# Performance work log

Measured on AMD Instinct MI355X. Metric: run time of the kernel, lower is better.

## Reference

```python
import jax, jax.numpy as jnp
import numpy as np
import math

B, N, DIM = 2, 4096, 256
NUM_HEADS = 8
HEAD_DIM = DIM // NUM_HEADS
WINDOW = 7  # default window_size in create_local_mask


def local_mask(seq_len: int, window_size: int = WINDOW) -> jnp.ndarray:
    """Boolean [N,N] mask: True where attention is allowed (2D grid locality)."""
    grid = int(math.isqrt(seq_len))
    idx = jnp.arange(seq_len)
    row, col = idx // grid, idx % grid
    half = window_size // 2
    ok_row = jnp.abs(row[:, None] - row[None, :]) <= half
    ok_col = jnp.abs(col[:, None] - col[None, :]) <= half
    return ok_row & ok_col


def setup_inputs() -> dict:
    key = jax.random.key(0)
    k1, k2, k3, k4 = jax.random.split(key, 4)
    x = jax.random.normal(k1, (B, N, DIM), dtype=jnp.float32)
    W_qkv = jax.random.normal(k2, (3 * DIM, DIM), dtype=jnp.float32) * (DIM ** -0.5)
    W_proj = jax.random.normal(k3, (DIM, DIM), dtype=jnp.float32) * (DIM ** -0.5)
    b_proj = jax.random.normal(k4, (DIM,), dtype=jnp.float32) * 0.01
    temperature = jnp.ones((1,), dtype=jnp.float32)
    return {"x": x, "W_qkv": W_qkv, "W_proj": W_proj, "b_proj": b_proj,
            "temperature": temperature}


def reference(x, W_qkv, W_proj, b_proj, temperature):
    Bb, Nn, C = x.shape
    scale = HEAD_DIM ** -0.5
    # qkv linear (no bias): [B,N,3C] -> [3,B,H,N,hd]
    qkv = (x @ W_qkv.T).reshape(Bb, Nn, 3, NUM_HEADS, HEAD_DIM)
    qkv = jnp.transpose(qkv, (2, 0, 3, 1, 4))
    q, k, v = qkv[0], qkv[1], qkv[2]
    # scores with learnable temperature
    attn = jnp.einsum('bhqd,bhkd->bhqk', q, k) * (scale * temperature[0])
    mask = local_mask(Nn)  # training path: N > 100 -> mask applied
    attn = jnp.where(mask[None, None, :, :], attn, -jnp.inf)
    attn = jax.nn.softmax(attn, axis=-1)
    out = jnp.einsum('bhqk,bhkd->bhqd', attn, v)  # [B,H,N,hd]
    out = jnp.transpose(out, (0, 2, 1, 3)).reshape(Bb, Nn, C)
    return out @ W_proj.T + b_proj
```

## Files before the change

### kernel.cpp

```cpp
#include <hip/hip_runtime.h>
#include <hip/hip_bf16.h>
#include <math.h>

#define DIM   256
#define NHEAD 8
#define HD    32
#define NTOK  4096
#define GRD   64
#define BATCH 2
#define MTOT  (BATCH * NTOK)
#define PLANE (NTOK * HD)

typedef __attribute__((ext_vector_type(8))) short bf16x8;
typedef __attribute__((ext_vector_type(4))) float f32x4;

static __device__ __forceinline__ unsigned short f2b(float f) {
  __hip_bfloat16 h = __float2bfloat16(f);
  union { __hip_bfloat16 h; unsigned short u; } cv;
  cv.h = h;
  return cv.u;
}

static __device__ __forceinline__ unsigned cvtpk_bf16(float lo, float hi) {
  unsigned r;
  asm("v_cvt_pk_bf16_f32 %0, %1, %2" : "=v"(r) : "v"(lo), "v"(hi));
  return r;
}

static __device__ __forceinline__ bf16x8 pack8(float4 a0, float4 a1) {
  union { bf16x8 v; unsigned short u[8]; } o;
  o.u[0] = f2b(a0.x); o.u[1] = f2b(a0.y); o.u[2] = f2b(a0.z); o.u[3] = f2b(a0.w);
  o.u[4] = f2b(a1.x); o.u[5] = f2b(a1.y); o.u[6] = f2b(a1.z); o.u[7] = f2b(a1.w);
  return o.v;
}

#define GLDS16(SRC, DST) __builtin_amdgcn_global_load_lds( \
    (const __attribute__((address_space(1))) void*)(SRC),  \
    (__attribute__((address_space(3))) void*)(DST), 16, 0, 0)

__global__ __launch_bounds__(256) void gemm_qkv(const float* __restrict__ A,
                                                const float* __restrict__ Bw,
                                                unsigned short* __restrict__ Cout) {
  const int K = 256;
  __shared__ __align__(16) char smem[34816];
  __hip_bfloat16* As = (__hip_bfloat16*)smem;
  __hip_bfloat16* Bs = (__hip_bfloat16*)(smem + 10240);
  const int tid = threadIdx.x;
  const int l = tid & 63, w = tid >> 6;
  const int bm = blockIdx.y * 128, bn = blockIdx.x * 128;
  const int wr = w >> 1, wc = w & 1;
  const int lr = l & 15, kh = l >> 4;
  const int lrow = l >> 2, lcol = (l & 3) * 8;

  f32x4 acc[4][4];
  #pragma unroll
  for (int i = 0; i < 4; ++i)
    #pragma unroll
    for (int j = 0; j < 4; ++j)
      acc[i][j] = (f32x4){0.f, 0.f, 0.f, 0.f};

  for (int k0 = 0; k0 < K; k0 += 32) {
    #pragma unroll
    for (int i = 0; i < 2; ++i) {
      const int r0 = (w * 2 + i) * 16;
      const float* ga = A  + (size_t)(bm + r0 + lrow) * K + k0 + lcol;
      const float* gb = Bw + (size_t)(bn + r0 + lrow) * K + k0 + lcol;
      float4 a0 = *(const float4*)ga, a1 = *(const float4*)(ga + 4);
      float4 b0 = *(const float4*)gb, b1 = *(const float4*)(gb + 4);
      *(bf16x8*)&As[(r0 + lrow) * 40 + lcol] = pack8(a0, a1);
      *(bf16x8*)&Bs[(r0 + lrow) * 40 + lcol] = pack8(b0, b1);
    }
    __syncthreads();

    bf16x8 af[4], bfr[4];
    #pragma unroll
    for (int f = 0; f < 4; ++f) {
      af[f]  = *(const bf16x8*)&As[(wr * 64 + f * 16 + lr) * 40 + kh * 8];
      bfr[f] = *(const bf16x8*)&Bs[(wc * 64 + f * 16 + lr) * 40 + kh * 8];
    }
    #pragma unroll
    for (int fi = 0; fi < 4; ++fi)
      #pragma unroll
      for (int fj = 0; fj < 4; ++fj)
        acc[fi][fj] = __builtin_amdgcn_mfma_f32_16x16x32_bf16(af[fi], bfr[fj], acc[fi][fj], 0, 0, 0);
    __syncthreads();
  }

  if (blockIdx.x < 4) {
    #pragma unroll
    for (int fi = 0; fi < 4; ++fi)
      #pragma unroll
      for (int fj = 0; fj < 4; ++fj)
        #pragma unroll
        for (int rr = 0; rr < 4; ++rr) {
          const int m = bm + wr * 64 + fi * 16 + kh * 4 + rr;
          const int n = bn + wc * 64 + fj * 16 + lr;
          const int sel = n >> 8, rem = n & 255;
          const int hh = rem >> 5, d = rem & 31;
          const int bb = m >> 12, tok = m & 4095;
          Cout[(size_t)(sel * 16 + bb * 8 + hh) * PLANE + tok * 32 + d] =
              f2b(acc[fi][fj][rr]);
        }
  } else {
    unsigned short* Ts = (unsigned short*)smem;
    #pragma unroll
    for (int fi = 0; fi < 4; ++fi)
      #pragma unroll
      for (int fj = 0; fj < 4; ++fj)
        #pragma unroll
        for (int rr = 0; rr < 4; ++rr) {
          const int tokl = wr * 64 + fi * 16 + kh * 4 + rr;
          const int dl   = wc * 64 + fj * 16 + lr;
          Ts[tokl * 136 + dl] = f2b(acc[fi][fj][rr]);
        }
    __syncthreads();
    const int dl = tid >> 1, th = (tid & 1) * 64;
    const int dg = (bn - 512) + dl;
    const int hh = dg >> 5, dd = dg & 31;
    const int bb = bm >> 12, tokb = bm & 4095;
    unsigned short* vt = Cout + (size_t)(32 + bb * 8 + hh) * PLANE + dd * 4096 + tokb + th;
    #pragma unroll
    for (int j = 0; j < 8; ++j) {
      union { bf16x8 v; unsigned short u[8]; } o;
      #pragma unroll
      for (int e = 0; e < 8; ++e)
        o.u[e] = Ts[(th + j * 8 + e) * 136 + dl];
      *(bf16x8*)(vt + j * 8) = o.v;
    }
  }
}

__global__ __launch_bounds__(256) void gemm_proj(const __hip_bfloat16* __restrict__ A,
                                                 const float* __restrict__ Bw,
                                                 const float* __restrict__ bias,
                                                 float* __restrict__ Cout) {
  const int K = 256, N = 256;
  __shared__ __hip_bfloat16 As[128 * 32];
  __shared__ __hip_bfloat16 Bs[128 * 40];
  const int tid = threadIdx.x;
  const int l = tid & 63, w = tid >> 6;
  const int bm = blockIdx.y * 128, bn = blockIdx.x * 128;
  const int wr = w >> 1, wc = w & 1;
  const int lr = l & 15, kh = l >> 4;
  const int lrow = l >> 2, lcol = (l & 3) * 8;

  f32x4 acc[4][4];
  #pragma unroll
  for (int i = 0; i < 4; ++i)
    #pragma unroll
    for (int j = 0; j < 4; ++j)
      acc[i][j] = (f32x4){0.f, 0.f, 0.f, 0.f};

  for (int k0 = 0; k0 < K; k0 += 32) {
    #pragma unroll
    for (int i = 0; i < 2; ++i) {
      const int r0 = (w * 2 + i) * 16;
      const __hip_bfloat16* ga = A + (size_t)(bm + r0 + lrow) * K + k0 + lcol;
      GLDS16(ga, &As[r0 * 32]);
      const float* gb = Bw + (size_t)(bn + r0 + lrow) * K + k0 + lcol;
      float4 b0 = *(const float4*)gb, b1 = *(const float4*)(gb + 4);
      *(bf16x8*)&Bs[(r0 + lrow) * 40 + lcol] = pack8(b0, b1);
    }
    __syncthreads();

    bf16x8 af[4], bfr[4];
    #pragma unroll
    for (int f = 0; f < 4; ++f) {
      af[f]  = *(const bf16x8*)&As[(wr * 64 + f * 16 + lr) * 32 + kh * 8];
      bfr[f] = *(const bf16x8*)&Bs[(wc * 64 + f * 16 + lr) * 40 + kh * 8];
    }
    #pragma unroll
    for (int fi = 0; fi < 4; ++fi)
      #pragma unroll
      for (int fj = 0; fj < 4; ++fj)
        acc[fi][fj] = __builtin_amdgcn_mfma_f32_16x16x32_bf16(af[fi], bfr[fj], acc[fi][fj], 0, 0, 0);
    __syncthreads();
  }

  #pragma unroll
  for (int fi = 0; fi < 4; ++fi)
    #pragma unroll
    for (int fj = 0; fj < 4; ++fj)
      #pragma unroll
      for (int rr = 0; rr < 4; ++rr) {
        const int m = bm + wr * 64 + fi * 16 + kh * 4 + rr;
        const int n = bn + wc * 64 + fj * 16 + lr;
        Cout[(size_t)m * N + n] = acc[fi][fj][rr] + bias[n];
      }
}

__global__ __launch_bounds__(256) void local_attn_mfma(
    const unsigned short* __restrict__ qkv, const float* __restrict__ temp,
    unsigned short* __restrict__ attn_out) {
  __shared__ __align__(16) unsigned short Ks[448 * 32];
  __shared__ __align__(16) unsigned short Vt[32 * 512];

  const int P = blockIdx.x;
  const int L = (P & 7) * 128 + (P >> 3);
  const int b = L >> 9, h = (L >> 6) & 7, r = L & 63;
  const int tid = threadIdx.x;
  const int l = tid & 63, wv = tid >> 6;
  const int q15 = l & 15, sg = l >> 4;

  const float scale = 0.17677669529663687f * temp[0];

  const unsigned short* qplane  = qkv + (size_t)(b * 8 + h) * PLANE;
  const unsigned short* kplane  = qplane + (size_t)16 * PLANE;
  const unsigned short* vtplane = qplane + (size_t)32 * PLANE;

  #pragma unroll
  for (int i = 0; i < 7; ++i) {
    const int ch = i * 256 + tid;
    const int tok = ch >> 2, jjp = ch & 3;
    const int ri = tok >> 6, kloc = tok & 63;
    int rr = r - 3 + ri; rr = rr < 0 ? 0 : (rr > 63 ? 63 : rr);
    const int jl = jjp ^ ((tok >> 1) & 3);
    const unsigned short* src = kplane + (size_t)(rr * 64 + kloc) * 32 + jl * 8;
    GLDS16(src, &Ks[(i * 256 + (tid & ~63)) * 8]);
  }
  #pragma unroll
  for (int i = 0; i < 8; ++i) {
    const int ch = i * 256 + tid;
    const int d = ch >> 6, chp = ch & 63;
    const int chl = chp ^ (d & 7);
    const int ri = chl >> 3, part = chl & 7;
    int rr = r - 3 + ri; rr = rr < 0 ? 0 : (rr > 63 ? 63 : rr);
    const unsigned short* src = vtplane + (size_t)d * 4096 + rr * 64 + part * 8;
    GLDS16(src, &Vt[(i * 256 + (tid & ~63)) * 8]);
  }

  const bf16x8 qf = *(const bf16x8*)(qplane + (size_t)(r * 64 + wv * 16 + q15) * 32 + sg * 8);

  __syncthreads();

  const int qcol = wv * 16 + q15;
  float m_run = -INFINITY, l_run = 0.f;
  f32x4 Od[2];
  Od[0] = (f32x4){0.f, 0.f, 0.f, 0.f};
  Od[1] = (f32x4){0.f, 0.f, 0.f, 0.f};
  const f32x4 zf = {0.f, 0.f, 0.f, 0.f};
  const int laA = ((l >> 4) & 1) * 32 + q15;
  const int laB = laA + 16;
  const bool hiG = (l & 32) != 0;

  #pragma unroll
  for (int c = 0; c < 7; ++c) {
    const int rr_c = r - 3 + c;
    if (rr_c >= 0 && rr_c <= 63) {
      f32x4 st[4];
      #pragma unroll
      for (int kt = 0; kt < 4; ++kt) {
        const int tok = c * 64 + kt * 16 + q15;
        const bf16x8 kf = *(const bf16x8*)((const char*)Ks + tok * 64 +
                                           ((sg ^ ((tok >> 1) & 3)) << 4));
        st[kt] = __builtin_amdgcn_mfma_f32_16x16x32_bf16(kf, qf, zf, 0, 0, 0);
      }
      float mc = -INFINITY;
      #pragma unroll
      for (int kt = 0; kt < 4; ++kt)
        #pragma unroll
        for (int rg = 0; rg < 4; ++rg) {
          const int keyloc = kt * 16 + sg * 4 + rg;
          const bool ok = (unsigned)(keyloc - qcol + 3) <= 6u;
          const float v = ok ? st[kt][rg] * scale : -INFINITY;
          st[kt][rg] = v;
          mc = fmaxf(mc, v);
        }
      mc = fmaxf(mc, __shfl_xor(mc, 16));
      mc = fmaxf(mc, __shfl_xor(mc, 32));
      const float mnew = fmaxf(m_run, mc);
      const float alpha = __expf(m_run - mnew);
      float lc = 0.f;
      #pragma unroll
      for (int kt = 0; kt < 4; ++kt)
        #pragma unroll
        for (int rg = 0; rg < 4; ++rg) {
          const float e = __expf(st[kt][rg] - mnew);
          st[kt][rg] = e;
          lc += e;
        }
      lc += __shfl_xor(lc, 16);
      lc += __shfl_xor(lc, 32);
      l_run = l_run * alpha + lc;
      m_run = mnew;
      Od[0] *= alpha;
      Od[1] *= alpha;

      unsigned pkw[8];
      #pragma unroll
      for (int kt = 0; kt < 4; ++kt) {
        pkw[kt * 2 + 0] = cvtpk_bf16(st[kt][0], st[kt][1]);
        pkw[kt * 2 + 1] = cvtpk_bf16(st[kt][2], st[kt][3]);
      }
      #pragma unroll
      for (int hf = 0; hf < 2; ++hf) {
        unsigned wA[2], wB[2];
        #pragma unroll
        for (int w2 = 0; w2 < 2; ++w2) {
          const unsigned a0 = (unsigned)__shfl((int)pkw[(2 * hf) * 2 + w2], laA);
          const unsigned a1 = (unsigned)__shfl((int)pkw[(2 * hf + 1) * 2 + w2], laA);
          wA[w2] = hiG ? a1 : a0;
          const unsigned b0 = (unsigned)__shfl((int)pkw[(2 * hf) * 2 + w2], laB);
          const unsigned b1 = (unsigned)__shfl((int)pkw[(2 * hf + 1) * 2 + w2], laB);
          wB[w2] = hiG ? b1 : b0;
        }
        union { unsigned u[4]; bf16x8 v; } pf;
        pf.u[0] = wA[0]; pf.u[1] = wA[1]; pf.u[2] = wB[0]; pf.u[3] = wB[1];
        #pragma unroll
        for (int dt = 0; dt < 2; ++dt) {
          const int d = dt * 16 + q15;
          const int chl = c * 8 + hf * 4 + sg;
          const bf16x8 vf = *(const bf16x8*)((const char*)Vt + d * 1024 +
                                             ((chl ^ (d & 7)) << 4));
          Od[dt] = __builtin_amdgcn_mfma_f32_16x16x32_bf16(vf, pf.v, Od[dt], 0, 0, 0);
        }
      }
    }
  }

  const float invl = 1.0f / l_run;
  #pragma unroll
  for (int dt = 0; dt < 2; ++dt) {
    const unsigned w0 = cvtpk_bf16(Od[dt][0] * invl, Od[dt][1] * invl);
    const unsigned w1 = cvtpk_bf16(Od[dt][2] * invl, Od[dt][3] * invl);
    unsigned short* dst = attn_out + (size_t)(b * 4096 + r * 64 + qcol) * 256 +
                          h * 32 + dt * 16 + sg * 4;
    uint2 uu; uu.x = w0; uu.y = w1;
    *(uint2*)dst = uu;
  }
}

extern "C" void kernel_launch(void* const* d_in, const int* in_sizes, int n_in,
                              void* d_out, int out_size, void* d_ws, size_t ws_size,
                              hipStream_t stream) {
  const float* x     = (const float*)d_in[0];
  const float* Wqkv  = (const float*)d_in[1];
  const float* Wproj = (const float*)d_in[2];
  const float* bproj = (const float*)d_in[3];
  const float* temp  = (const float*)d_in[4];
  float* out = (float*)d_out;

  char* ws = (char*)d_ws;
  unsigned short* qkv_bf  = (unsigned short*)ws;
  __hip_bfloat16* attn_bf = (__hip_bfloat16*)(ws + 25165824);

  {
    dim3 grid(3 * DIM / 128, MTOT / 128);
    gemm_qkv<<<grid, 256, 0, stream>>>(x, Wqkv, qkv_bf);
  }
  local_attn_mfma<<<BATCH * NHEAD * GRD, 256, 0, stream>>>(qkv_bf, temp,
                                                           (unsigned short*)attn_bf);
  {
    dim3 grid(DIM / 128, MTOT / 128);
    gemm_proj<<<grid, 256, 0, stream>>>(attn_bf, Wproj, bproj, out);
  }
}
```

Before: 50.64 us.

## Process two query rows per attention block and shrink proj GEMM M-tile

The attention kernel now uses 512-thread blocks that each handle two adjacent query grid rows and share a single 8-row K/V window in LDS. Previously each 256-thread block loaded its own 7-row window, so this cuts redundant global loads and halves the grid. The output projection GEMM switches from 128-row to 64-row tiles, doubling its block count so more CUs are busy on the small problem. The cost is more LDS per attention block and less operand reuse per proj block.

```diff
diff --git a/kernel.cpp b/kernel.cpp
--- a/kernel.cpp
+++ b/kernel.cpp
@@ -135,42 +135,45 @@
                                                  const float* __restrict__ bias,
                                                  float* __restrict__ Cout) {
   const int K = 256, N = 256;
-  __shared__ __hip_bfloat16 As[128 * 32];
+  __shared__ __hip_bfloat16 As[64 * 32];
   __shared__ __hip_bfloat16 Bs[128 * 40];
   const int tid = threadIdx.x;
   const int l = tid & 63, w = tid >> 6;
-  const int bm = blockIdx.y * 128, bn = blockIdx.x * 128;
+  const int bm = blockIdx.y * 64, bn = blockIdx.x * 128;
   const int wr = w >> 1, wc = w & 1;
   const int lr = l & 15, kh = l >> 4;
-  const int lrow = l >> 2, lcol = (l & 3) * 8;
-
-  f32x4 acc[4][4];
-  #pragma unroll
-  for (int i = 0; i < 4; ++i)
+  const int lrow = tid >> 2, lcol = (tid & 3) * 8;
+
+  f32x4 acc[2][4];
+  #pragma unroll
+  for (int i = 0; i < 2; ++i)
     #pragma unroll
     for (int j = 0; j < 4; ++j)
       acc[i][j] = (f32x4){0.f, 0.f, 0.f, 0.f};
 
   for (int k0 = 0; k0 < K; k0 += 32) {
+    {
+      const __hip_bfloat16* ga = A + (size_t)(bm + lrow) * K + k0 + lcol;
+      GLDS16(ga, &As[w * 512]);
+    }
     #pragma unroll
     for (int i = 0; i < 2; ++i) {
-      const int r0 = (w * 2 + i) * 16;
-      const __hip_bfloat16* ga = A + (size_t)(bm + r0 + lrow) * K + k0 + lcol;
-      GLDS16(ga, &As[r0 * 32]);
-      const float* gb = Bw + (size_t)(bn + r0 + lrow) * K + k0 + lcol;
+      const int row = i * 64 + lrow;
+      const float* gb = Bw + (size_t)(bn + row) * K + k0 + lcol;
       float4 b0 = *(const float4*)gb, b1 = *(const float4*)(gb + 4);
-      *(bf16x8*)&Bs[(r0 + lrow) * 40 + lcol] = pack8(b0, b1);
-    }
-    __syncthreads();
-
-    bf16x8 af[4], bfr[4];
-    #pragma unroll
-    for (int f = 0; f < 4; ++f) {
-      af[f]  = *(const bf16x8*)&As[(wr * 64 + f * 16 + lr) * 32 + kh * 8];
+      *(bf16x8*)&Bs[row * 40 + lcol] = pack8(b0, b1);
+    }
+    __syncthreads();
+
+    bf16x8 af[2], bfr[4];
+    #pragma unroll
+    for (int f = 0; f < 2; ++f)
+      af[f] = *(const bf16x8*)&As[(wr * 32 + f * 16 + lr) * 32 + kh * 8];
+    #pragma unroll
+    for (int f = 0; f < 4; ++f)
       bfr[f] = *(const bf16x8*)&Bs[(wc * 64 + f * 16 + lr) * 40 + kh * 8];
-    }
-    #pragma unroll
-    for (int fi = 0; fi < 4; ++fi)
+    #pragma unroll
+    for (int fi = 0; fi < 2; ++fi)
       #pragma unroll
       for (int fj = 0; fj < 4; ++fj)
         acc[fi][fj] = __builtin_amdgcn_mfma_f32_16x16x32_bf16(af[fi], bfr[fj], acc[fi][fj], 0, 0, 0);
@@ -178,29 +181,32 @@
   }
 
   #pragma unroll
-  for (int fi = 0; fi < 4; ++fi)
+  for (int fi = 0; fi < 2; ++fi)
     #pragma unroll
     for (int fj = 0; fj < 4; ++fj)
       #pragma unroll
       for (int rr = 0; rr < 4; ++rr) {
-        const int m = bm + wr * 64 + fi * 16 + kh * 4 + rr;
+        const int m = bm + wr * 32 + fi * 16 + kh * 4 + rr;
         const int n = bn + wc * 64 + fj * 16 + lr;
         Cout[(size_t)m * N + n] = acc[fi][fj][rr] + bias[n];
       }
 }
 
-__global__ __launch_bounds__(256) void local_attn_mfma(
+__global__ __launch_bounds__(512, 4) void local_attn_mfma(
     const unsigned short* __restrict__ qkv, const float* __restrict__ temp,
     unsigned short* __restrict__ attn_out) {
-  __shared__ __align__(16) unsigned short Ks[448 * 32];
+  __shared__ __align__(16) unsigned short Ks[512 * 32];
   __shared__ __align__(16) unsigned short Vt[32 * 512];
 
   const int P = blockIdx.x;
-  const int L = (P & 7) * 128 + (P >> 3);
-  const int b = L >> 9, h = (L >> 6) & 7, r = L & 63;
+  const int L = (P & 7) * 64 + (P >> 3);
+  const int plane = L >> 5, rp = L & 31;
+  const int b = plane >> 3, h = plane & 7;
   const int tid = threadIdx.x;
   const int l = tid & 63, wv = tid >> 6;
+  const int qr = wv >> 2, wq = wv & 3;
   const int q15 = l & 15, sg = l >> 4;
+  const int r = rp * 2 + qr;
 
   const float scale = 0.17677669529663687f * temp[0];
 
@@ -208,32 +214,34 @@
   const unsigned short* kplane  = qplane + (size_t)16 * PLANE;
   const unsigned short* vtplane = qplane + (size_t)32 * PLANE;
 
-  #pragma unroll
-  for (int i = 0; i < 7; ++i) {
-    const int ch = i * 256 + tid;
+  const int rbase = rp * 2 - 3;
+
+  #pragma unroll
+  for (int i = 0; i < 4; ++i) {
+    const int ch = i * 512 + tid;
     const int tok = ch >> 2, jjp = ch & 3;
     const int ri = tok >> 6, kloc = tok & 63;
-    int rr = r - 3 + ri; rr = rr < 0 ? 0 : (rr > 63 ? 63 : rr);
+    int row = rbase + ri; row = row < 0 ? 0 : (row > 63 ? 63 : row);
     const int jl = jjp ^ ((tok >> 1) & 3);
-    const unsigned short* src = kplane + (size_t)(rr * 64 + kloc) * 32 + jl * 8;
-    GLDS16(src, &Ks[(i * 256 + (tid & ~63)) * 8]);
-  }
-  #pragma unroll
-  for (int i = 0; i < 8; ++i) {
-    const int ch = i * 256 + tid;
+    const unsigned short* src = kplane + (size_t)(row * 64 + kloc) * 32 + jl * 8;
+    GLDS16(src, &Ks[(i * 512 + (tid & ~63)) * 8]);
+  }
+  #pragma unroll
+  for (int i = 0; i < 4; ++i) {
+    const int ch = i * 512 + tid;
     const int d = ch >> 6, chp = ch & 63;
     const int chl = chp ^ (d & 7);
     const int ri = chl >> 3, part = chl & 7;
-    int rr = r - 3 + ri; rr = rr < 0 ? 0 : (rr > 63 ? 63 : rr);
-    const unsigned short* src = vtplane + (size_t)d * 4096 + rr * 64 + part * 8;
-    GLDS16(src, &Vt[(i * 256 + (tid & ~63)) * 8]);
-  }
-
-  const bf16x8 qf = *(const bf16x8*)(qplane + (size_t)(r * 64 + wv * 16 + q15) * 32 + sg * 8);
+    int row = rbase + ri; row = row < 0 ? 0 : (row > 63 ? 63 : row);
+    const unsigned short* src = vtplane + (size_t)d * 4096 + row * 64 + part * 8;
+    GLDS16(src, &Vt[(i * 512 + (tid & ~63)) * 8]);
+  }
+
+  const bf16x8 qf = *(const bf16x8*)(qplane + (size_t)(r * 64 + wq * 16 + q15) * 32 + sg * 8);
 
   __syncthreads();
 
-  const int qcol = wv * 16 + q15;
+  const int qcol = wq * 16 + q15;
   float m_run = -INFINITY, l_run = 0.f;
   f32x4 Od[2];
   Od[0] = (f32x4){0.f, 0.f, 0.f, 0.f};
@@ -247,10 +255,11 @@
   for (int c = 0; c < 7; ++c) {
     const int rr_c = r - 3 + c;
     if (rr_c >= 0 && rr_c <= 63) {
+      const int bri = c + qr;
       f32x4 st[4];
       #pragma unroll
       for (int kt = 0; kt < 4; ++kt) {
-        const int tok = c * 64 + kt * 16 + q15;
+        const int tok = bri * 64 + kt * 16 + q15;
         const bf16x8 kf = *(const bf16x8*)((const char*)Ks + tok * 64 +
                                            ((sg ^ ((tok >> 1) & 3)) << 4));
         st[kt] = __builtin_amdgcn_mfma_f32_16x16x32_bf16(kf, qf, zf, 0, 0, 0);
@@ -309,7 +318,7 @@
         #pragma unroll
         for (int dt = 0; dt < 2; ++dt) {
           const int d = dt * 16 + q15;
-          const int chl = c * 8 + hf * 4 + sg;
+          const int chl = bri * 8 + hf * 4 + sg;
           const bf16x8 vf = *(const bf16x8*)((const char*)Vt + d * 1024 +
                                              ((chl ^ (d & 7)) << 4));
           Od[dt] = __builtin_amdgcn_mfma_f32_16x16x32_bf16(vf, pf.v, Od[dt], 0, 0, 0);
@@ -348,10 +357,10 @@
     dim3 grid(3 * DIM / 128, MTOT / 128);
     gemm_qkv<<<grid, 256, 0, stream>>>(x, Wqkv, qkv_bf);
   }
-  local_attn_mfma<<<BATCH * NHEAD * GRD, 256, 0, stream>>>(qkv_bf, temp,
-                                                           (unsigned short*)attn_bf);
+  local_attn_mfma<<<BATCH * NHEAD * (GRD / 2), 512, 0, stream>>>(
+      qkv_bf, temp, (unsigned short*)attn_bf);
   {
-    dim3 grid(DIM / 128, MTOT / 128);
+    dim3 grid(DIM / 128, MTOT / 64);
     gemm_proj<<<grid, 256, 0, stream>>>(attn_bf, Wproj, bproj, out);
   }
 }
```

Measured after the change: 45.92 us. -9.3%, faster.
